# Performance work log

Hardware: AMD Instinct MI355X
Metric: run time of the kernel (lower is better)

Reference implementation:

```python
import jax, jax.numpy as jnp
import numpy as np

TAU = 2.0
V_TH = 0.5
BN_EPS = 1e-5
ALPHA = 2.0  # spikingjelly surrogate.ATan default

@jax.custom_vjp
def spike_fn(x):
    # Heaviside forward, ATan surrogate backward (defined for fwdbwd parity)
    return (x >= 0.0).astype(x.dtype)

def _spike_fwd(x):
    return spike_fn(x), x

def _spike_bwd(x, g):
    return (g * (ALPHA / 2.0) / (1.0 + (jnp.pi / 2.0 * ALPHA * x) ** 2),)

spike_fn.defvjp(_spike_fwd, _spike_bwd)

def lif_multistep(x_seq):
    # MultiStepLIFNode: v <- v + (x - v)/tau ; spike = H(v - v_th) ; hard reset v<-v*(1-sg(spike))
    def step(v, x_t):
        v = v + (x_t - v) / TAU
        s = spike_fn(v - V_TH)
        v = v * (1.0 - jax.lax.stop_gradient(s))  # detach_reset=True, v_reset=0
        return v, s
    v0 = jnp.zeros_like(x_seq[0])
    _, spikes = jax.lax.scan(step, v0, x_seq)
    return spikes

def setup_inputs() -> dict:
    key = jax.random.key(0)
    k1, k2, k3 = jax.random.split(key, 3)
    T, B, N, D = 4, 64, 256, 512
    x = jax.random.normal(k1, (T, B, N, D), jnp.float32)
    mx = jax.random.normal(k2, (N, B, T, D), jnp.float32)
    W = jax.random.normal(k3, (D, D), jnp.float32) / np.sqrt(D).astype(np.float32)
    gamma = jnp.ones((D,), jnp.float32)
    beta = jnp.zeros((D,), jnp.float32)
    return {"x": x, "mx": mx, "W": W, "gamma": gamma, "beta": beta}

def reference(x, mx, W, gamma, beta):
    # mx: [N,B,T,D] -> transpose(0,2) -> [T,B,N,D]
    mxt = jnp.transpose(mx, (2, 1, 0, 3))
    # Linear (no bias): [T,B,N,D] @ W^T
    h = jnp.einsum('tbnd,ed->tbne', mxt, W)
    # BatchNorm1d(D) in training mode: stats over (T*B, N) per channel D (biased var)
    mean = h.mean(axis=(0, 1, 2))
    var = h.var(axis=(0, 1, 2))
    hn = (h - mean) * jax.lax.rsqrt(var + BN_EPS) * gamma + beta
    # LIF recurrence over T
    s = lif_multistep(hn)  # [T,B,N,D] binary spikes
    return x * s
```

## Files before the change

kernel.cpp:

```cpp
#include <hip/hip_runtime.h>
#include <math.h>

namespace {
constexpr int TDIM = 4, BDIM = 64, NDIM = 256, DDIM = 512;
constexpr int MROWS = 65536;
constexpr long long BND = 8388608LL;
constexpr double BN_EPS = 1e-5;

constexpr int BM = 64, BNT = 128, BK = 32;
constexpr int APITCH = BK + 2;
constexpr int WPITCH = BNT + 4;
constexpr int LDS_BYTES = (BM * APITCH + BK * WPITCH) * 8;

constexpr int BM3 = 128, BN3 = 64, BK3 = 16;
constexpr int AP3 = BM3 + 1;
constexpr int WP3 = BN3 + 1;

constexpr int NSA = 6, NSW = 5;
constexpr long long APL = 33554432LL;
constexpr long long WPL = 262144LL;
constexpr int CH8 = 22528;
}

typedef double d4 __attribute__((ext_vector_type(4)));
typedef int i32x4 __attribute__((ext_vector_type(4)));
typedef int i32x16 __attribute__((ext_vector_type(16)));

#define GLOAD16(g, d) __builtin_amdgcn_global_load_lds( \
    (const __attribute__((address_space(1))) void*)(g), \
    (__attribute__((address_space(3))) void*)(d), 16, 0, 0)

__global__ void probe_k(double* __restrict__ rowmap)
{
    const int l = threadIdx.x;
    d4 z = {0.0, 0.0, 0.0, 0.0};
    d4 dr = __builtin_amdgcn_mfma_f64_16x16x4f64((double)(l & 15), 1.0, z, 0, 0, 0);
#pragma unroll
    for (int r = 0; r < 4; ++r)
        rowmap[l * 4 + r] = dr[r] * 0.25;
}

__global__ void probe8_k(double* __restrict__ irow8, double* __restrict__ icol8)
{
    const int l = threadIdx.x;
    i32x16 z;
#pragma unroll
    for (int r = 0; r < 16; ++r) z[r] = 0;
    const int mb = (l & 31) * 0x01010101;
    const int ob = 0x01010101;
    i32x4 am = {mb, mb, mb, mb};
    i32x4 a1 = {ob, ob, ob, ob};
    i32x16 d1 = __builtin_amdgcn_mfma_i32_32x32x32_i8(am, a1, z, 0, 0, 0);
#pragma unroll
    for (int r = 0; r < 16; ++r)
        irow8[l * 16 + r] = (double)d1[r] / 32.0;
    i32x16 d2 = __builtin_amdgcn_mfma_i32_32x32x32_i8(a1, am, z, 0, 0, 0);
    icol8[l] = (double)d2[0] / 32.0;
}

__global__ __launch_bounds__(256)
void slice_a_k(const float* __restrict__ src, char* __restrict__ dst)
{
    const int ri  = threadIdx.x & 63;
    const int ks0 = threadIdx.x >> 6;
    const long long row = (long long)blockIdx.x * 64 + ri;
#pragma unroll 1
    for (int it = 0; it < 8; ++it) {
        const int kseg = it * 4 + ks0;
        const float* sp = src + row * DDIM + kseg * 16;
        union { char c[16]; i32x4 v; } pk[NSA];
#pragma unroll
        for (int e = 0; e < 16; ++e) {
            double V = (double)sp[e] * 4.0;
            double u = rint(V);
            double r = V - u;
            pk[0].c[e] = (char)(int)u;
#pragma unroll
            for (int s = 1; s < NSA; ++s) {
                r *= 128.0;
                u = rint(r);
                r -= u;
                pk[s].c[e] = (char)(int)u;
            }
        }
        const long long base = (long long)blockIdx.x * 32768 + kseg * 1024 + ri * 16;
#pragma unroll
        for (int s = 0; s < NSA; ++s)
            *(i32x4*)(dst + (long long)s * APL + base) = pk[s].v;
    }
}

__global__ __launch_bounds__(256)
void slice_w_k(const float* __restrict__ src, char* __restrict__ dst)
{
    const int cbk  = blockIdx.x >> 3;
    const int kgrp = blockIdx.x & 7;
    const int ci   = threadIdx.x & 63;
    const int kseg = kgrp * 4 + (threadIdx.x >> 6);
    const float* sp = src + (long long)(cbk * 64 + ci) * DDIM + kseg * 16;
    union { char c[16]; i32x4 v; } pk[NSW];
#pragma unroll
    for (int e = 0; e < 16; ++e) {
        double V = (double)sp[e] * 256.0;
        double u = rint(V);
        double r = V - u;
        pk[0].c[e] = (char)(int)u;
#pragma unroll
        for (int s = 1; s < NSW; ++s) {
            r *= 128.0;
            u = rint(r);
            r -= u;
            pk[s].c[e] = (char)(int)u;
        }
    }
    const long long base = (long long)cbk * 32768 + kseg * 1024 + ci * 16;
#pragma unroll
    for (int s = 0; s < NSW; ++s)
        *(i32x4*)(dst + (long long)s * WPL + base) = pk[s].v;
}

template<int NW>
struct Stager {
    const char* gp[NW];
    int lo[NW];
    __device__ __forceinline__ void init(int w0, const char* Asl, const char* Wsl,
                                         long long aT, long long wT, int l)
    {
#pragma unroll
        for (int i = 0; i < NW; ++i) {
            const int idx = w0 + i;
            if (idx < 12) {
                gp[i] = Asl + (long long)(idx >> 1) * APL + aT
                      + (long long)(idx & 1) * 1024 + l * 16;
                lo[i] = (idx >> 1) * 2048 + (idx & 1) * 1024;
            } else {
                const int e = idx - 12;
                gp[i] = Wsl + (long long)(e >> 1) * WPL + wT
                      + (long long)(e & 1) * 1024 + l * 16;
                lo[i] = 12288 + (e >> 1) * 2048 + (e & 1) * 1024;
            }
        }
    }
    __device__ __forceinline__ void issue(char* buf)
    {
#pragma unroll
        for (int i = 0; i < NW; ++i) {
            GLOAD16(gp[i], buf + lo[i]);
            gp[i] += 2048;
        }
    }
};

template<int NW>
__device__ __forceinline__ void gemm8_loop(Stager<NW>& st, char* smb,
                                           i32x16 (&acc)[6], int roA, int roW)
{
#pragma unroll 2
    for (int c = 0; c < 16; ++c) {
        const char* bA = smb + (c & 1) * CH8;
        const char* bW = bA + 12288;
        i32x4 af[NSA], wf[NSW];
#pragma unroll
        for (int s = 0; s < NSA; ++s)
            af[s] = *(const i32x4*)(bA + s * 2048 + roA);
#pragma unroll
        for (int t = 0; t < NSW; ++t)
            wf[t] = *(const i32x4*)(bW + t * 2048 + roW);
#pragma unroll
        for (int s = 0; s < NSA; ++s)
#pragma unroll
            for (int t = 0; t < NSW; ++t)
                if (s + t <= 5)
                    acc[s + t] = __builtin_amdgcn_mfma_i32_32x32x32_i8(
                                     af[s], wf[t], acc[s + t], 0, 0, 0);
        if (c == 15) break;
        asm volatile("s_barrier" ::: "memory");
        if (c < 14) {
            st.issue(smb + (c & 1) * CH8);
            if constexpr (NW == 6)
                asm volatile("s_waitcnt vmcnt(6)" ::: "memory");
            else
                asm volatile("s_waitcnt vmcnt(5)" ::: "memory");
        } else {
            asm volatile("s_waitcnt vmcnt(0)" ::: "memory");
        }
        __builtin_amdgcn_sched_barrier(0);
        asm volatile("s_barrier" ::: "memory");
        __builtin_amdgcn_sched_barrier(0);
    }
}

__global__ __launch_bounds__(256, 3)
void gemm8_k(const char* __restrict__ Asl, const char* __restrict__ Wsl,
             double* __restrict__ hbuf, double* __restrict__ sums,
             const double* __restrict__ irow8, const double* __restrict__ icol8)
{
    __shared__ __align__(16) char sm[2][CH8];

    const int tid = threadIdx.x;
    const int bid = blockIdx.x;
    const int rb  = ((bid >> 6) << 3) | (bid & 7);
    const int cb  = (bid >> 3) & 7;

    const int w  = tid >> 6;
    const int l  = tid & 63;
    const int wr = w >> 1;
    const int wc = w & 1;

    const long long aTile = (long long)rb * 32768;
    const long long wTile = (long long)cb * 32768;

    i32x16 acc[6];
#pragma unroll
    for (int g = 0; g < 6; ++g)
#pragma unroll
        for (int r = 0; r < 16; ++r) acc[g][r] = 0;

    const int roA = (l >> 5) * 1024 + (32 * wr + (l & 31)) * 16;
    const int roW = (l >> 5) * 1024 + (32 * wc + (l & 31)) * 16;

    char* smb = &sm[0][0];
    if (w < 2) {
        Stager<6> st;
        st.init(6 * w, Asl, Wsl, aTile, wTile, l);
        st.issue(smb);
        st.issue(smb + CH8);
        asm volatile("s_waitcnt vmcnt(6)" ::: "memory");
        __builtin_amdgcn_sched_barrier(0);
        asm volatile("s_barrier" ::: "memory");
        __builtin_amdgcn_sched_barrier(0);
        gemm8_loop<6>(st, smb, acc, roA, roW);
    } else {
        Stager<5> st;
        st.init(12 + 5 * (w - 2), Asl, Wsl, aTile, wTile, l);
        st.issue(smb);
        st.issue(smb + CH8);
        asm volatile("s_waitcnt vmcnt(5)" ::: "memory");
        __builtin_amdgcn_sched_barrier(0);
        asm volatile("s_barrier" ::: "memory");
        __builtin_amdgcn_sched_barrier(0);
        gemm8_loop<5>(st, smb, acc, roA, roW);
    }

    int irw[16];
#pragma unroll
    for (int r = 0; r < 16; ++r) irw[r] = (int)irow8[l * 16 + r];
    const int icl = (int)icol8[l];

    const double C7 = 1.0 / 128.0, CMB = 1.0 / 1024.0;
    double lsum = 0.0, lsq = 0.0;
    const int colg = cb * 64 + 32 * wc + icl;
    const int row0 = rb * 64 + 32 * wr;
#pragma unroll
    for (int r = 0; r < 16; ++r) {
        double t = (double)acc[5][r];
        t = fma(t, C7, (double)acc[4][r]);
        t = fma(t, C7, (double)acc[3][r]);
        t = fma(t, C7, (double)acc[2][r]);
        t = fma(t, C7, (double)acc[1][r]);
        t = fma(t, C7, (double)acc[0][r]);
        const double h = t * CMB;
        hbuf[(size_t)(row0 + irw[r]) * DDIM + colg] = h;
        lsum += h;
        lsq = fma(h, h, lsq);
    }

    __syncthreads();
    double* Ss = (double*)sm;
    const int ctr = wr * 2 + (l >> 5);
    const int cloc = 32 * wc + icl;
    Ss[cloc * 4 + ctr] = lsum;
    Ss[256 + cloc * 4 + ctr] = lsq;
    __syncthreads();
    if (tid < 64) {
        double s = 0.0, q = 0.0;
#pragma unroll
        for (int k = 0; k < 4; ++k) {
            s += Ss[tid * 4 + k];
            q += Ss[256 + tid * 4 + k];
        }
        atomicAdd(&sums[cb * 64 + tid], s);
        atomicAdd(&sums[512 + cb * 64 + tid], q);
    }
}

__global__ __launch_bounds__(256, 2)
void gemm3_k(const float* __restrict__ mx, const float* __restrict__ Wm,
             double* __restrict__ hbuf, double* __restrict__ sums,
             const double* __restrict__ rowmap)
{
    __shared__ double Atr[BK3 * AP3];
    __shared__ double Wt [BK3 * WP3];

    const int tid = threadIdx.x;
    const int bid = blockIdx.x;
    const int rb  = ((bid >> 6) << 3) | (bid & 7);
    const int cb  = (bid >> 3) & 7;
    const int row0 = rb * BM3;
    const int col0 = cb * BN3;

    const int w  = tid >> 6;
    const int l  = tid & 63;
    const int wr = w >> 1;
    const int wc = w & 1;
    const int lr = l & 15;
    const int kq = l >> 4;

    int irow[4];
#pragma unroll
    for (int r = 0; r < 4; ++r)
        irow[r] = (int)rowmap[l * 4 + r];

    const int arow = tid >> 1;
    const int af   = (tid & 1) * 8;
    const int wrow = tid >> 2;
    const int wf   = (tid & 3) * 4;
    const float* aSrc = mx + (size_t)(row0 + arow) * DDIM + af;
    const float* wSrc = Wm + (size_t)(col0 + wrow) * DDIM + wf;

    d4 acc[4][2];
#pragma unroll
    for (int i = 0; i < 4; ++i)
#pragma unroll
        for (int j = 0; j < 2; ++j) acc[i][j] = (d4){0.0, 0.0, 0.0, 0.0};

    float4 pa0 = *(const float4*)(aSrc + 0);
    float4 pa1 = *(const float4*)(aSrc + 4);
    float4 pw  = *(const float4*)(wSrc + 0);

    for (int kk = 0; kk < DDIM; kk += BK3) {
        __syncthreads();
        Atr[(af + 0) * AP3 + arow] = (double)pa0.x;
        Atr[(af + 1) * AP3 + arow] = (double)pa0.y;
        Atr[(af + 2) * AP3 + arow] = (double)pa0.z;
        Atr[(af + 3) * AP3 + arow] = (double)pa0.w;
        Atr[(af + 4) * AP3 + arow] = (double)pa1.x;
        Atr[(af + 5) * AP3 + arow] = (double)pa1.y;
        Atr[(af + 6) * AP3 + arow] = (double)pa1.z;
        Atr[(af + 7) * AP3 + arow] = (double)pa1.w;
        Wt[(wf + 0) * WP3 + wrow] = (double)pw.x;
        Wt[(wf + 1) * WP3 + wrow] = (double)pw.y;
        Wt[(wf + 2) * WP3 + wrow] = (double)pw.z;
        Wt[(wf + 3) * WP3 + wrow] = (double)pw.w;
        __syncthreads();

        if (kk + BK3 < DDIM) {
            pa0 = *(const float4*)(aSrc + kk + BK3 + 0);
            pa1 = *(const float4*)(aSrc + kk + BK3 + 4);
            pw  = *(const float4*)(wSrc + kk + BK3 + 0);
        }

#pragma unroll
        for (int ks = 0; ks < BK3 / 4; ++ks) {
            const int kabs = ks * 4 + kq;
            double a[4], b[2];
#pragma unroll
            for (int i = 0; i < 4; ++i)
                a[i] = Atr[kabs * AP3 + 64 * wr + 16 * i + lr];
#pragma unroll
            for (int j = 0; j < 2; ++j)
                b[j] = Wt[kabs * WP3 + 32 * wc + 16 * j + lr];
#pragma unroll
            for (int i = 0; i < 4; ++i)
#pragma unroll
                for (int j = 0; j < 2; ++j)
                    acc[i][j] = __builtin_amdgcn_mfma_f64_16x16x4f64(
                                    a[i], b[j], acc[i][j], 0, 0, 0);
        }
    }

#pragma unroll
    for (int i = 0; i < 4; ++i) {
#pragma unroll
        for (int j = 0; j < 2; ++j) {
            const size_t cbase = (size_t)col0 + 32 * wc + 16 * j + lr;
            const size_t rbase = (size_t)row0 + 64 * wr + 16 * i;
#pragma unroll
            for (int r = 0; r < 4; ++r)
                hbuf[(rbase + irow[r]) * DDIM + cbase] = acc[i][j][r];
        }
    }

    __syncthreads();
    double* Ssum = Atr;
    double* Ssq  = Atr + 512;
    const int ctr = wr * 4 + kq;
#pragma unroll
    for (int j = 0; j < 2; ++j) {
        const int cloc = 32 * wc + 16 * j + lr;
        double s = 0.0, q = 0.0;
#pragma unroll
        for (int i = 0; i < 4; ++i)
#pragma unroll
            for (int r = 0; r < 4; ++r) {
                const double v = acc[i][j][r];
                s += v;
                q = fma(v, v, q);
            }
        Ssum[cloc * 8 + ctr] = s;
        Ssq [cloc * 8 + ctr] = q;
    }
    __syncthreads();
    if (tid < 64) {
        double s = 0.0, q = 0.0;
#pragma unroll
        for (int c = 0; c < 8; ++c) {
            s += Ssum[tid * 8 + c];
            q += Ssq [tid * 8 + c];
        }
        atomicAdd(&sums[col0 + tid], s);
        atomicAdd(&sums[512 + col0 + tid], q);
    }
}

template<int MODE>
__global__ __launch_bounds__(256)
void gemm_k(const float* __restrict__ mx, const float* __restrict__ Wm,
            double* __restrict__ hbuf, double* __restrict__ sums,
            const double* __restrict__ scale, const double* __restrict__ shiftv,
            const float* __restrict__ x, float* __restrict__ out)
{
    __shared__ __align__(16) char smem[LDS_BYTES];
    double (*Ald)[APITCH] = reinterpret_cast<double(*)[APITCH]>(smem);
    double (*Wld)[WPITCH] = reinterpret_cast<double(*)[WPITCH]>(smem + (size_t)BM * APITCH * 8);

    const int tid  = threadIdx.x;
    const int rb   = blockIdx.x >> 2;
    const int cb   = blockIdx.x & 3;
    const int row0 = rb * BM;
    const int col0 = cb * BNT;

    const int arow = tid >> 2;
    const int ak   = (tid & 3) * 8;
    const int erow = tid >> 1;
    const int wk   = (tid & 1) * 16;

    const float* aSrc = mx + (size_t)(row0 + arow) * DDIM;
    const float* wSrc = Wm + (size_t)(col0 + erow) * DDIM;

    const int rg = tid >> 4;
    const int cg = tid & 15;

    double acc[4][8];
#pragma unroll
    for (int i = 0; i < 4; ++i)
#pragma unroll
        for (int j = 0; j < 8; ++j) acc[i][j] = 0.0;

    for (int kk = 0; kk < DDIM; kk += BK) {
        const float4 a0 = *(const float4*)(aSrc + kk + ak);
        const float4 a1 = *(const float4*)(aSrc + kk + ak + 4);
        const float4 w0 = *(const float4*)(wSrc + kk + wk);
        const float4 w1 = *(const float4*)(wSrc + kk + wk + 4);
        const float4 w2 = *(const float4*)(wSrc + kk + wk + 8);
        const float4 w3 = *(const float4*)(wSrc + kk + wk + 12);
        __syncthreads();
        Ald[arow][ak + 0] = (double)a0.x; Ald[arow][ak + 1] = (double)a0.y;
        Ald[arow][ak + 2] = (double)a0.z; Ald[arow][ak + 3] = (double)a0.w;
        Ald[arow][ak + 4] = (double)a1.x; Ald[arow][ak + 5] = (double)a1.y;
        Ald[arow][ak + 6] = (double)a1.z; Ald[arow][ak + 7] = (double)a1.w;
        const float wfv[16] = {w0.x, w0.y, w0.z, w0.w, w1.x, w1.y, w1.z, w1.w,
                               w2.x, w2.y, w2.z, w2.w, w3.x, w3.y, w3.z, w3.w};
#pragma unroll
        for (int q = 0; q < 16; ++q) Wld[wk + q][erow] = (double)wfv[q];
        __syncthreads();

#pragma unroll 4
        for (int d = 0; d < BK; ++d) {
            double a[4], wv[8];
#pragma unroll
            for (int i = 0; i < 4; ++i) a[i] = Ald[rg * 4 + i][d];
#pragma unroll
            for (int j = 0; j < 8; ++j) wv[j] = Wld[d][cg * 8 + j];
#pragma unroll
            for (int i = 0; i < 4; ++i)
#pragma unroll
                for (int j = 0; j < 8; ++j)
                    acc[i][j] = fma(a[i], wv[j], acc[i][j]);
        }
    }

    if (MODE <= 1) {
        __syncthreads();
        double* scr = reinterpret_cast<double*>(smem);
#pragma unroll
        for (int j = 0; j < 8; ++j) {
            const double s = acc[0][j] + acc[1][j] + acc[2][j] + acc[3][j];
            const double q = acc[0][j]*acc[0][j] + acc[1][j]*acc[1][j]
                           + acc[2][j]*acc[2][j] + acc[3][j]*acc[3][j];
            scr[(cg * 8 + j) * 16 + rg] = s;
            scr[2048 + (cg * 8 + j) * 16 + rg] = q;
        }
        __syncthreads();
        if (tid < 128) {
            double s = 0.0, q = 0.0;
#pragma unroll
            for (int r = 0; r < 16; ++r) {
                s += scr[tid * 16 + r];
                q += scr[2048 + tid * 16 + r];
            }
            atomicAdd(&sums[col0 + tid], s);
            atomicAdd(&sums[512 + col0 + tid], q);
        }
    }

    if (MODE == 2) {
        const int p  = rb * 16 + rg;
        const int nn = p >> 6;
        const int bb = p & 63;
#pragma unroll
        for (int j = 0; j < 8; ++j) {
            const int e = col0 + cg * 8 + j;
            const double sc = scale[e];
            const double sh = shiftv[e];
            const size_t basex = (size_t)bb * (NDIM * DDIM) + (size_t)nn * DDIM + e;
            double v = 0.0;
#pragma unroll
            for (int t = 0; t < 4; ++t) {
                const double hn = fma(acc[t][j], sc, sh);
                v = v + (hn - v) / 2.0;
                const bool s = (v - 0.5) >= 0.0;
                const size_t xi = (size_t)t * BND + basex;
                out[xi] = s ? x[xi] : 0.0f;
                if (s) v = 0.0;
            }
        }
    }
}

__global__ void zero_k(double* sums)
{
    const int i = blockIdx.x * 256 + threadIdx.x;
    if (i < 1024) sums[i] = 0.0;
}

__global__ void stat_k(const double* __restrict__ sums,
                       const float* __restrict__ gamma, const float* __restrict__ beta,
                       double* __restrict__ scale, double* __restrict__ shiftv)
{
    const int e = blockIdx.x * 256 + threadIdx.x;
    if (e < 512) {
        const double mean = sums[e] * (1.0 / 65536.0);
        const double msq  = sums[512 + e] * (1.0 / 65536.0);
        const double var  = msq - mean * mean;
        const double inv  = 1.0 / sqrt(var + BN_EPS);
        const double g    = (double)gamma[e] * inv;
        scale[e]  = g;
        shiftv[e] = (double)beta[e] - mean * g;
    }
}

__global__ __launch_bounds__(256)
void lifh_k(const double* __restrict__ hbuf, const double* __restrict__ scale,
            const double* __restrict__ shiftv, const float* __restrict__ x,
            float* __restrict__ out)
{
    const size_t i = (size_t)blockIdx.x * 256 + threadIdx.x;
    const int e  = (int)(i & 511);
    const size_t p = i >> 9;
    const int nn = (int)(p >> 6);
    const int bb = (int)(p & 63);
    const double sc = scale[e];
    const double sh = shiftv[e];
    const double* hp = hbuf + p * 2048 + e;
    const size_t basex = (size_t)bb * (NDIM * DDIM) + (size_t)nn * DDIM + e;
    double v = 0.0;
#pragma unroll
    for (int t = 0; t < 4; ++t) {
        const double hn = fma(hp[(size_t)t * 512], sc, sh);
        v = v + (hn - v) / 2.0;
        const bool s = (v - 0.5) >= 0.0;
        const size_t xi = (size_t)t * BND + basex;
        out[xi] = s ? x[xi] : 0.0f;
        if (s) v = 0.0;
    }
}

extern "C" void kernel_launch(void* const* d_in, const int* in_sizes, int n_in,
                              void* d_out, int out_size, void* d_ws, size_t ws_size,
                              hipStream_t stream)
{
    const float* x     = (const float*)d_in[0];
    const float* mx    = (const float*)d_in[1];
    const float* Wm    = (const float*)d_in[2];
    const float* gamma = (const float*)d_in[3];
    const float* beta  = (const float*)d_in[4];
    float* out = (float*)d_out;

    char* ws = (char*)d_ws;
    double* sums   = (double*)ws;
    double* scale  = (double*)(ws + 8192);
    double* shiftv = scale + 512;
    double* rowmap = (double*)(ws + 16384);
    double* irow8  = (double*)(ws + 18432);
    double* icol8  = (double*)(ws + 26624);
    double* hbuf   = (double*)(ws + 32768);

    const size_t HBSZ   = (size_t)MROWS * DDIM * 8;
    const size_t OFF_AS = 32768 + HBSZ;
    const size_t ASSZ   = (size_t)NSA * APL;
    const size_t OFF_WS = OFF_AS + ASSZ;
    const size_t WSSZ   = (size_t)NSW * WPL;
    const size_t need8  = OFF_WS + WSSZ;
    const size_t need_h = 32768 + HBSZ;

    hipLaunchKernelGGL(zero_k, dim3(4), dim3(256), 0, stream, sums);

    if (ws_size >= need8) {
        char* Asl = ws + OFF_AS;
        char* Wsl = ws + OFF_WS;
        hipLaunchKernelGGL(probe8_k, dim3(1), dim3(64), 0, stream, irow8, icol8);
        hipLaunchKernelGGL(slice_a_k, dim3(1024), dim3(256), 0, stream, mx, Asl);
        hipLaunchKernelGGL(slice_w_k, dim3(64), dim3(256), 0, stream, Wm, Wsl);
        hipLaunchKernelGGL(gemm8_k, dim3(8192), dim3(256), 0, stream,
                           Asl, Wsl, hbuf, sums, irow8, icol8);
        hipLaunchKernelGGL(stat_k, dim3(2), dim3(256), 0, stream,
                           sums, gamma, beta, scale, shiftv);
        hipLaunchKernelGGL(lifh_k, dim3(32768), dim3(256), 0, stream,
                           hbuf, scale, shiftv, x, out);
    } else if (ws_size >= need_h) {
        hipLaunchKernelGGL(probe_k, dim3(1), dim3(64), 0, stream, rowmap);
        hipLaunchKernelGGL(gemm3_k, dim3(4096), dim3(256), 0, stream,
                           mx, Wm, hbuf, sums, rowmap);
        hipLaunchKernelGGL(stat_k, dim3(2), dim3(256), 0, stream,
                           sums, gamma, beta, scale, shiftv);
        hipLaunchKernelGGL(lifh_k, dim3(32768), dim3(256), 0, stream,
                           hbuf, scale, shiftv, x, out);
    } else {
        hipLaunchKernelGGL((gemm_k<0>), dim3(4096), dim3(256), 0, stream,
                           mx, Wm, nullptr, sums, nullptr, nullptr, nullptr, nullptr);
        hipLaunchKernelGGL(stat_k, dim3(2), dim3(256), 0, stream,
                           sums, gamma, beta, scale, shiftv);
        hipLaunchKernelGGL((gemm_k<2>), dim3(4096), dim3(256), 0, stream,
                           mx, Wm, nullptr, nullptr, scale, shiftv, x, out);
    }
}
```

Measured before the change: 480.0 us.

## Use fp32 for residual slicing, reorder LDS loads with setprio, vectorize LIF kernel

The slicing kernels now compute the residual digit extraction in fp32 instead of fp64 after the first digit, which cuts slow double-precision ALU work. The int8 GEMM loop loads the first A slice before the W slices and raises wave priority around the MFMA block. The LIF kernel processes two channels per thread with double2 and float2 vector loads and stores, and runs on half the grid. The fp32 residual may lose exactness in the lower digits, which would change the emulated fp64 product.

```diff
diff --git a/kernel.cpp b/kernel.cpp
--- a/kernel.cpp
+++ b/kernel.cpp
@@ -71,16 +71,16 @@
         union { char c[16]; i32x4 v; } pk[NSA];
 #pragma unroll
         for (int e = 0; e < 16; ++e) {
-            double V = (double)sp[e] * 4.0;
-            double u = rint(V);
-            double r = V - u;
+            const double V = (double)sp[e] * 4.0;
+            const double u = rint(V);
             pk[0].c[e] = (char)(int)u;
+            float r = (float)(V - u);
 #pragma unroll
             for (int s = 1; s < NSA; ++s) {
-                r *= 128.0;
-                u = rint(r);
-                r -= u;
-                pk[s].c[e] = (char)(int)u;
+                r *= 128.0f;
+                const float uf = rintf(r);
+                r -= uf;
+                pk[s].c[e] = (char)(int)uf;
             }
         }
         const long long base = (long long)blockIdx.x * 32768 + kseg * 1024 + ri * 16;
@@ -101,16 +101,16 @@
     union { char c[16]; i32x4 v; } pk[NSW];
 #pragma unroll
     for (int e = 0; e < 16; ++e) {
-        double V = (double)sp[e] * 256.0;
-        double u = rint(V);
-        double r = V - u;
+        const double V = (double)sp[e] * 256.0;
+        const double u = rint(V);
         pk[0].c[e] = (char)(int)u;
+        float r = (float)(V - u);
 #pragma unroll
         for (int s = 1; s < NSW; ++s) {
-            r *= 128.0;
-            u = rint(r);
-            r -= u;
-            pk[s].c[e] = (char)(int)u;
+            r *= 128.0f;
+            const float uf = rintf(r);
+            r -= uf;
+            pk[s].c[e] = (char)(int)uf;
         }
     }
     const long long base = (long long)cbk * 32768 + kseg * 1024 + ci * 16;
@@ -160,12 +160,14 @@
         const char* bA = smb + (c & 1) * CH8;
         const char* bW = bA + 12288;
         i32x4 af[NSA], wf[NSW];
-#pragma unroll
-        for (int s = 0; s < NSA; ++s)
-            af[s] = *(const i32x4*)(bA + s * 2048 + roA);
+        af[0] = *(const i32x4*)(bA + roA);
 #pragma unroll
         for (int t = 0; t < NSW; ++t)
             wf[t] = *(const i32x4*)(bW + t * 2048 + roW);
+#pragma unroll
+        for (int s = 1; s < NSA; ++s)
+            af[s] = *(const i32x4*)(bA + s * 2048 + roA);
+        __builtin_amdgcn_s_setprio(1);
 #pragma unroll
         for (int s = 0; s < NSA; ++s)
 #pragma unroll
@@ -173,6 +175,7 @@
                 if (s + t <= 5)
                     acc[s + t] = __builtin_amdgcn_mfma_i32_32x32x32_i8(
                                      af[s], wf[t], acc[s + t], 0, 0, 0);
+        __builtin_amdgcn_s_setprio(0);
         if (c == 15) break;
         asm volatile("s_barrier" ::: "memory");
         if (c < 14) {
@@ -556,23 +559,32 @@
             float* __restrict__ out)
 {
     const size_t i = (size_t)blockIdx.x * 256 + threadIdx.x;
-    const int e  = (int)(i & 511);
-    const size_t p = i >> 9;
+    const int e2 = (int)(i & 255) * 2;
+    const size_t p = i >> 8;
     const int nn = (int)(p >> 6);
     const int bb = (int)(p & 63);
-    const double sc = scale[e];
-    const double sh = shiftv[e];
-    const double* hp = hbuf + p * 2048 + e;
-    const size_t basex = (size_t)bb * (NDIM * DDIM) + (size_t)nn * DDIM + e;
-    double v = 0.0;
+    const double2 sc = *(const double2*)&scale[e2];
+    const double2 sh = *(const double2*)&shiftv[e2];
+    const double* hp = hbuf + p * 2048 + e2;
+    const size_t basex = (size_t)bb * (NDIM * DDIM) + (size_t)nn * DDIM + e2;
+    double v0 = 0.0, v1 = 0.0;
 #pragma unroll
     for (int t = 0; t < 4; ++t) {
-        const double hn = fma(hp[(size_t)t * 512], sc, sh);
-        v = v + (hn - v) / 2.0;
-        const bool s = (v - 0.5) >= 0.0;
+        const double2 h2 = *(const double2*)(hp + (size_t)t * 512);
+        const double hn0 = fma(h2.x, sc.x, sh.x);
+        const double hn1 = fma(h2.y, sc.y, sh.y);
+        v0 = v0 + (hn0 - v0) / 2.0;
+        v1 = v1 + (hn1 - v1) / 2.0;
+        const bool s0 = (v0 - 0.5) >= 0.0;
+        const bool s1 = (v1 - 0.5) >= 0.0;
         const size_t xi = (size_t)t * BND + basex;
-        out[xi] = s ? x[xi] : 0.0f;
-        if (s) v = 0.0;
+        const float2 xv = *(const float2*)(x + xi);
+        float2 ov;
+        ov.x = s0 ? xv.x : 0.0f;
+        ov.y = s1 ? xv.y : 0.0f;
+        *(float2*)(out + xi) = ov;
+        if (s0) v0 = 0.0;
+        if (s1) v1 = 0.0;
     }
 }
 
@@ -616,7 +628,7 @@
                            Asl, Wsl, hbuf, sums, irow8, icol8);
         hipLaunchKernelGGL(stat_k, dim3(2), dim3(256), 0, stream,
                            sums, gamma, beta, scale, shiftv);
-        hipLaunchKernelGGL(lifh_k, dim3(32768), dim3(256), 0, stream,
+        hipLaunchKernelGGL(lifh_k, dim3(16384), dim3(256), 0, stream,
                            hbuf, scale, shiftv, x, out);
     } else if (ws_size >= need_h) {
         hipLaunchKernelGGL(probe_k, dim3(1), dim3(64), 0, stream, rowmap);
@@ -624,7 +636,7 @@
                            mx, Wm, hbuf, sums, rowmap);
         hipLaunchKernelGGL(stat_k, dim3(2), dim3(256), 0, stream,
                            sums, gamma, beta, scale, shiftv);
-        hipLaunchKernelGGL(lifh_k, dim3(32768), dim3(256), 0, stream,
+        hipLaunchKernelGGL(lifh_k, dim3(16384), dim3(256), 0, stream,
                            hbuf, scale, shiftv, x, out);
     } else {
         hipLaunchKernelGGL((gemm_k<0>), dim3(4096), dim3(256), 0, stream,
```

New measurement: 510.4 us. 6.3% more time.
